# Kernel optimization log

Measured on AMD Instinct MI355X. Metric: run time of the kernel, lower is better.

The kernel has to match this reference:

```python
import jax, jax.numpy as jnp
import numpy as np
import math

INNER = 96
EPS = 1e-8  # torch CosineSimilarity eps


def _proj(x, W1, W2):
    # nn.Linear(C,C,bias=False) -> ReLU -> nn.Linear(C,inner,bias=False)
    return jax.nn.relu(x @ W1) @ W2


def _cos(a, b):
    # torch CosineSimilarity(dim=-1): dot / (max(||a||,eps)*max(||b||,eps))
    num = jnp.sum(a * b, axis=-1)
    na = jnp.maximum(jnp.linalg.norm(a, axis=-1), EPS)
    nb = jnp.maximum(jnp.linalg.norm(b, axis=-1), EPS)
    return num / (na * nb)


def setup_inputs() -> dict:
    key = jax.random.key(0)
    ks = jax.random.split(key, 8)
    B, C, H, W = 128, 768, 7, 7
    sc1 = 1.0 / math.sqrt(C)
    inp = {
        "features_a": jax.random.normal(ks[0], (B, C, H, W), jnp.float32),
        "features_b": jax.random.normal(ks[1], (B, C, H, W), jnp.float32),
        "Wq1": jax.random.normal(ks[2], (C, C), jnp.float32) * sc1,
        "Wq2": jax.random.normal(ks[3], (C, INNER), jnp.float32) * sc1,
        "Wk1": jax.random.normal(ks[4], (C, C), jnp.float32) * sc1,
        "Wk2": jax.random.normal(ks[5], (C, INNER), jnp.float32) * sc1,
        "Wv1": jax.random.normal(ks[6], (C, C), jnp.float32) * sc1,
        "Wv2": jax.random.normal(ks[7], (C, INNER), jnp.float32) * sc1,
    }
    return inp


def reference(features_a, features_b, Wq1, Wq2, Wk1, Wk2, Wv1, Wv2):
    B, C = features_a.shape[0], features_a.shape[1]
    # [B, C, H, W] -> [B, S, C]
    fa = features_a.reshape(B, C, -1).transpose(0, 2, 1)
    fb = features_b.reshape(features_b.shape[0], C, -1).transpose(0, 2, 1)

    qa, ka, va = _proj(fa, Wq1, Wq2), _proj(fa, Wk1, Wk2), _proj(fa, Wv1, Wv2)
    qb, kb, vb = _proj(fb, Wq1, Wq2), _proj(fb, Wk1, Wk2), _proj(fb, Wv1, Wv2)

    scale = 1.0 / math.sqrt(INNER)

    # query_b vs key_a: [Bb, Ba, Sq, Sk]
    scores_ba = jnp.einsum('bqe,ake->baqk', qb, ka) * scale
    probs_ba = jax.nn.softmax(scores_ba, axis=-1)
    aligned_a = jnp.einsum('baqk,ake->baqe', probs_ba, va)  # [Bb, Ba, S, inner]

    # query_a vs key_b: [Bb, Ba, Sq, Sk]
    scores_ab = jnp.einsum('aqe,bke->baqk', qa, kb) * scale
    probs_ab = jax.nn.softmax(scores_ab, axis=-1)
    aligned_b = jnp.einsum('baqk,bke->baqe', probs_ab, vb)  # [Bb, Ba, S, inner]

    sim = _cos(va[None, :, :, :], aligned_b) + _cos(vb[:, None, :, :], aligned_a)
    return sim.mean(-1)  # [Bb, Ba]
```

## Files before the change

kernel.cpp:

```cpp
#include <hip/hip_runtime.h>
#include <hip/hip_bf16.h>
#include <math.h>

typedef __attribute__((ext_vector_type(8))) short bf16x8;
typedef __attribute__((ext_vector_type(4))) float f32x4;

#define MROWS 12544
#define CDIM 768
#define INNER 96
#define S49 49
#define NSIDE 6272
#define SCALE 0.10206207261596577f
#define SCALE_EXP2 ((float)(0.10206207261596577 * 1.4426950408889634))

__device__ __forceinline__ unsigned short f2bf(float f) {
  union { float f; unsigned u; } v; v.f = f;
  unsigned u = v.u;
  return (unsigned short)((u + 0x7fffu + ((u >> 16) & 1u)) >> 16);
}
__device__ __forceinline__ float bf2f(unsigned short h) {
  union { unsigned u; float f; } v; v.u = ((unsigned)h) << 16;
  return v.f;
}
__device__ __forceinline__ unsigned pack_bf16_rn(float a, float b) {
  union { float f; unsigned u; } ua, ub; ua.f = a; ub.f = b;
  return __builtin_amdgcn_perm(ub.u + 0x8000u, ua.u + 0x8000u, 0x07060302u);
}

__device__ __forceinline__ void gld16(const unsigned short* g, unsigned short* l) {
  __builtin_amdgcn_global_load_lds(
      (const __attribute__((address_space(1))) unsigned int*)(g),
      (__attribute__((address_space(3))) unsigned int*)(l), 16, 0, 0);
}

__global__ __launch_bounds__(256) void prep_all(
    const float* __restrict__ fa, const float* __restrict__ fb,
    const float* __restrict__ w10, const float* __restrict__ w11,
    const float* __restrict__ w12, const float* __restrict__ w20,
    const float* __restrict__ w21, const float* __restrict__ w22,
    unsigned short* __restrict__ X,
    unsigned short* __restrict__ W1T, unsigned short* __restrict__ W2T,
    unsigned short* __restrict__ VtKpad) {
  const int t = threadIdx.x;
  int id = blockIdx.x;
  if (id < 3072) {
    __shared__ float T[64][50];
    const int z = id / 1536; id -= z * 1536;
    const int ct = id % 12, img = id / 12;
    const float* feat = z ? fb : fa;
    const float* src = feat + (size_t)img * (CDIM * S49) + (size_t)ct * 64 * S49;
    for (int idx = t; idx < 64 * S49; idx += 256) {
      int cc = idx / S49, s = idx - cc * S49;
      T[cc][s] = src[cc * S49 + s];
    }
    __syncthreads();
    unsigned short* dst = X + (size_t)(z * 128 + img) * S49 * CDIM + ct * 64;
    for (int idx = t; idx < S49 * 64; idx += 256) {
      int s = idx >> 6, cc = idx & 63;
      dst[(size_t)s * CDIM + cc] = f2bf(T[cc][s]);
    }
  } else if (id < 5016) {
    __shared__ float T[32][33];
    id -= 3072;
    const float* src;
    unsigned short* dst;
    int C, ctile, rtile;
    if (id < 1728) {
      int wdx = id / 576, tid = id - wdx * 576;
      ctile = tid % 24; rtile = tid / 24;
      src = wdx == 0 ? w10 : (wdx == 1 ? w11 : w12);
      dst = W1T + (size_t)wdx * CDIM * CDIM;
      C = CDIM;
    } else {
      id -= 1728;
      int wdx = id / 72, tid = id - wdx * 72;
      ctile = tid % 3; rtile = tid / 3;
      src = wdx == 0 ? w20 : (wdx == 1 ? w21 : w22);
      dst = W2T + (size_t)wdx * INNER * CDIM;
      C = INNER;
    }
    const int c0 = ctile * 32, r0 = rtile * 32;
    for (int idx = t; idx < 1024; idx += 256) {
      int rr = idx >> 5, cc = idx & 31;
      T[rr][cc] = src[(size_t)(r0 + rr) * C + c0 + cc];
    }
    __syncthreads();
    for (int idx = t; idx < 1024; idx += 256) {
      int rr = idx >> 5, cc = idx & 31;
      dst[(size_t)(c0 + rr) * CDIM + r0 + cc] = f2bf(T[cc][rr]);
    }
  } else {
    id -= 5016;
    ushort4* p4 = (ushort4*)VtKpad;
    const ushort4 z = make_ushort4(0, 0, 0, 0);
#pragma unroll
    for (int i = 0; i < 32; i++)
      p4[(size_t)id * 8192 + i * 256 + t] = z;
  }
}

__global__ __launch_bounds__(512) void gemm1b4(const unsigned short* __restrict__ X,
                                               const unsigned short* __restrict__ W1T,
                                               unsigned short* __restrict__ H,
                                               int wbase, int hsel) {
  __shared__ __align__(16) unsigned short As[128 * 64];
  __shared__ __align__(16) unsigned short Bs[128 * 64];
  const int t = threadIdx.x;
  const int lane = t & 63, w = t >> 6;
  const int lr = lane & 15, lq = lane >> 4;
  const int wm = w & 3;
  const int wn = w >> 2;
  const int m0 = blockIdx.y * 128, n0 = blockIdx.x * 128;
  const int wdx = blockIdx.z + wbase;
  const unsigned short* W1w = W1T + (size_t)wdx * CDIM * CDIM;
  unsigned short* Hw = H + (hsel ? (size_t)wdx * MROWS * CDIM : 0);
  const f32x4 z4 = {0.f, 0.f, 0.f, 0.f};
  f32x4 acc[2][4] = {{z4, z4, z4, z4}, {z4, z4, z4, z4}};

  for (int k0 = 0; k0 < CDIM; k0 += 64) {
    __syncthreads();
#pragma unroll
    for (int j = 0; j < 2; j++) {
      int idx = t + j * 512;
      int row = idx >> 3, col = (idx & 7) * 8;
      gld16(X + (size_t)(m0 + row) * CDIM + k0 + col, As + idx * 8);
      gld16(W1w + (size_t)(n0 + row) * CDIM + k0 + col, Bs + idx * 8);
    }
    __syncthreads();
#pragma unroll
    for (int ks = 0; ks < 2; ks++) {
      bf16x8 a[2], b[4];
#pragma unroll
      for (int mt = 0; mt < 2; mt++)
        a[mt] = *(const bf16x8*)(As + (wm * 32 + mt * 16 + lr) * 64 + ks * 32 + lq * 8);
#pragma unroll
      for (int nt = 0; nt < 4; nt++)
        b[nt] = *(const bf16x8*)(Bs + (wn * 64 + nt * 16 + lr) * 64 + ks * 32 + lq * 8);
#pragma unroll
      for (int mt = 0; mt < 2; mt++)
#pragma unroll
        for (int nt = 0; nt < 4; nt++)
          acc[mt][nt] = __builtin_amdgcn_mfma_f32_16x16x32_bf16(a[mt], b[nt], acc[mt][nt], 0, 0, 0);
    }
  }
#pragma unroll
  for (int mt = 0; mt < 2; mt++)
#pragma unroll
    for (int nt = 0; nt < 4; nt++)
#pragma unroll
      for (int r = 0; r < 4; r++) {
        int m = m0 + wm * 32 + mt * 16 + lq * 4 + r;
        int n = n0 + wn * 64 + nt * 16 + lr;
        Hw[(size_t)m * CDIM + n] = f2bf(fmaxf(acc[mt][nt][r], 0.f));
      }
}

#define LDK 72
__global__ __launch_bounds__(256) void gemm2b3(const unsigned short* __restrict__ H,
                                               const unsigned short* __restrict__ W2T,
                                               unsigned short* __restrict__ QKV,
                                               unsigned short* __restrict__ Kpad,
                                               unsigned short* __restrict__ Vt,
                                               float* __restrict__ vnorm,
                                               int wbase, int hsel) {
  __shared__ __align__(16) unsigned short As[64 * LDK];
  __shared__ __align__(16) unsigned short Bs[96 * LDK];
  const int t = threadIdx.x;
  const int lane = t & 63, w = t >> 6;
  const int lr = lane & 15, lq = lane >> 4;
  const int m0 = blockIdx.x * 64;
  const int wdx = blockIdx.y + wbase;
  const unsigned short* Hw = H + (hsel ? (size_t)wdx * MROWS * CDIM : 0);
  const unsigned short* W2w = W2T + (size_t)wdx * INNER * CDIM;
  const f32x4 z4 = {0.f, 0.f, 0.f, 0.f};
  f32x4 acc[6] = {z4, z4, z4, z4, z4, z4};

  for (int k0 = 0; k0 < CDIM; k0 += 64) {
    __syncthreads();
    for (int c = t; c < 512; c += 256) {
      int r = c >> 3, kc = (c & 7) * 8;
      *(uint4*)(As + r * LDK + kc) = *(const uint4*)(Hw + (size_t)(m0 + r) * CDIM + k0 + kc);
    }
    for (int c = t; c < 768; c += 256) {
      int r = c >> 3, kc = (c & 7) * 8;
      *(uint4*)(Bs + r * LDK + kc) = *(const uint4*)(W2w + (size_t)r * CDIM + k0 + kc);
    }
    __syncthreads();
#pragma unroll
    for (int kk = 0; kk < 2; kk++) {
      bf16x8 a = *(const bf16x8*)(As + (w * 16 + lr) * LDK + kk * 32 + lq * 8);
#pragma unroll
      for (int nt = 0; nt < 6; nt++) {
        bf16x8 b = *(const bf16x8*)(Bs + (nt * 16 + lr) * LDK + kk * 32 + lq * 8);
        acc[nt] = __builtin_amdgcn_mfma_f32_16x16x32_bf16(a, b, acc[nt], 0, 0, 0);
      }
    }
  }
  float nsq[4] = {0.f, 0.f, 0.f, 0.f};
#pragma unroll
  for (int nt = 0; nt < 6; nt++)
#pragma unroll
    for (int r = 0; r < 4; r++) {
      int m = m0 + w * 16 + lq * 4 + r;
      int e = nt * 16 + lr;
      float v = acc[nt][r];
      int img = m / 49, s = m - img * 49;
      if (wdx == 0) {
        QKV[(size_t)m * INNER + e] = f2bf(v * SCALE_EXP2);
      } else if (wdx == 1) {
        Kpad[(size_t)(img * 64 + s) * INNER + e] = f2bf(v);
      } else {
        QKV[(size_t)(2 * MROWS + m) * INNER + e] = f2bf(v);
        Vt[(size_t)img * (INNER * 64) + e * 64 + s] = f2bf(v);
        nsq[r] += v * v;
      }
    }
  if (wdx == 2) {
#pragma unroll
    for (int r = 0; r < 4; r++) {
      float p = nsq[r];
      p += __shfl_xor(p, 1, 16);
      p += __shfl_xor(p, 2, 16);
      p += __shfl_xor(p, 4, 16);
      p += __shfl_xor(p, 8, 16);
      if (lr == 0) vnorm[m0 + w * 16 + lq * 4 + r] = sqrtf(p);
    }
  }
}

__global__ __launch_bounds__(256) void attn9(const unsigned short* __restrict__ Qp,
                                             const unsigned short* __restrict__ Kpad,
                                             const unsigned short* __restrict__ V,
                                             const unsigned short* __restrict__ Vt,
                                             const float* __restrict__ vnorm,
                                             float* __restrict__ cosbuf) {
  __shared__ __align__(16) unsigned short KsD[2][64 * INNER];
  __shared__ __align__(16) unsigned short VtS[INNER * 64];
  __shared__ __align__(16) unsigned short Ps[4][32 * 64];

  const int t = threadIdx.x;
  const int lane = t & 63, w = t >> 6;
  const int lr = lane & 15, lq = lane >> 4;
  const f32x4 z4 = {0.f, 0.f, 0.f, 0.f};

  int bx = blockIdx.x;
  const int dir = bx / 392; bx -= dir * 392;
  const int chunk = bx >> 3, fg = bx & 7;
  const int r0 = chunk * 128;
  const int qbase = dir * NSIDE;

  int goK[3], goV[3], lo[3];
#pragma unroll
  for (int j = 0; j < 3; j++) {
    int l = (w * 3 + j) * 64 + lane;
    lo[j] = l * 8;
    int rK = l / 12, scK = l - rK * 12;
    int ccK = scK - ((rK >> 1) & 7); if (ccK < 0) ccK += 12;
    goK[j] = rK * INNER + ccK * 8;
    int rV = l >> 3, scV = l & 7;
    int ccV = (scV - (rV & 7)) & 7;
    goV[j] = rV * 64 + ccV * 8;
  }
  int rdK[3], rdV[2];
#pragma unroll
  for (int ks = 0; ks < 3; ks++) {
    int sc = (ks * 4 + lq + ((lr >> 1) & 7)) % 12;
    rdK[ks] = lr * INNER + sc * 8;
  }
#pragma unroll
  for (int ks = 0; ks < 2; ks++) {
    int sc = (ks * 4 + lq + (lr & 7)) & 7;
    rdV[ks] = lr * 64 + sc * 8;
  }

  bf16x8 qf[2][3];
#pragma unroll
  for (int qt = 0; qt < 2; qt++) {
    const int qrow = qbase + r0 + w * 32 + qt * 16 + lr;
#pragma unroll
    for (int ks = 0; ks < 3; ks++)
      qf[qt][ks] = *(const bf16x8*)(Qp + (size_t)qrow * INNER + ks * 32 + lq * 8);
  }
  float rv[2][6][4], invvn[2];
#pragma unroll
  for (int qt = 0; qt < 2; qt++) {
    const int qrow = qbase + r0 + w * 32 + qt * 16 + lr;
    invvn[qt] = 1.f / fmaxf(vnorm[qrow], 1e-8f);
#pragma unroll
    for (int et = 0; et < 6; et++) {
      ushort4 u = *(const ushort4*)(V + (size_t)qrow * INNER + et * 16 + lq * 4);
      rv[qt][et][0] = bf2f(u.x); rv[qt][et][1] = bf2f(u.y);
      rv[qt][et][2] = bf2f(u.z); rv[qt][et][3] = bf2f(u.w);
    }
  }

  unsigned short* Pw = &Ps[w][0];
  const int kimg0 = (dir == 0 ? 128 : 0) + fg * 16;
  {
    const unsigned short* kg = Kpad + (size_t)kimg0 * (64 * INNER);
#pragma unroll
    for (int j = 0; j < 3; j++) gld16(kg + goK[j], &KsD[0][0] + lo[j]);
  }
  for (int fi = 0; fi < 16; fi++) {
    const int f = fg * 16 + fi;
    __syncthreads();
    {
      const unsigned short* vg = Vt + (size_t)(kimg0 + fi) * (INNER * 64);
#pragma unroll
      for (int j = 0; j < 3; j++) gld16(vg + goV[j], VtS + lo[j]);
    }
    const unsigned short* KsC = &KsD[fi & 1][0];
    f32x4 s4[2][4] = {{z4, z4, z4, z4}, {z4, z4, z4, z4}};
#pragma unroll
    for (int ks = 0; ks < 3; ks++) {
#pragma unroll
      for (int kt = 0; kt < 4; kt++) {
        bf16x8 a = *(const bf16x8*)(KsC + kt * (16 * INNER) + rdK[ks]);
        s4[0][kt] = __builtin_amdgcn_mfma_f32_16x16x32_bf16(a, qf[0][ks], s4[0][kt], 0, 0, 0);
        s4[1][kt] = __builtin_amdgcn_mfma_f32_16x16x32_bf16(a, qf[1][ks], s4[1][kt], 0, 0, 0);
      }
    }
#pragma unroll
    for (int qt = 0; qt < 2; qt++)
#pragma unroll
      for (int kt = 0; kt < 4; kt++) {
        float e0 = __builtin_exp2f(s4[qt][kt][0]);
        float e1 = __builtin_exp2f(s4[qt][kt][1]);
        float e2 = __builtin_exp2f(s4[qt][kt][2]);
        float e3 = __builtin_exp2f(s4[qt][kt][3]);
        uint2 pk = make_uint2(pack_bf16_rn(e0, e1), pack_bf16_rn(e2, e3));
        int row = qt * 16 + lr;
        int ch = (2 * kt + (lq >> 1)) ^ (row & 7);
        *(uint2*)(Pw + row * 64 + ch * 8 + (lq & 1) * 4) = pk;
      }
    __syncthreads();
    if (fi < 15) {
      const unsigned short* kg = Kpad + (size_t)(kimg0 + fi + 1) * (64 * INNER);
      unsigned short* kd = &KsD[1 - (fi & 1)][0];
#pragma unroll
      for (int j = 0; j < 3; j++) gld16(kg + goK[j], kd + lo[j]);
    }
    f32x4 pv[2][6] = {{z4, z4, z4, z4, z4, z4}, {z4, z4, z4, z4, z4, z4}};
#pragma unroll
    for (int ks = 0; ks < 2; ks++) {
      int row0 = 0 * 16 + lr, row1 = 1 * 16 + lr;
      int ch0 = ((ks * 4 + lq) ^ (row0 & 7));
      int ch1 = ((ks * 4 + lq) ^ (row1 & 7));
      bf16x8 b0 = *(const bf16x8*)(Pw + row0 * 64 + ch0 * 8);
      bf16x8 b1 = *(const bf16x8*)(Pw + row1 * 64 + ch1 * 8);
#pragma unroll
      for (int et = 0; et < 6; et++) {
        bf16x8 a = *(const bf16x8*)(VtS + et * (16 * 64) + rdV[ks]);
        pv[0][et] = __builtin_amdgcn_mfma_f32_16x16x32_bf16(a, b0, pv[0][et], 0, 0, 0);
        pv[1][et] = __builtin_amdgcn_mfma_f32_16x16x32_bf16(a, b1, pv[1][et], 0, 0, 0);
      }
    }
#pragma unroll
    for (int qt = 0; qt < 2; qt++) {
      float d = 0.f, nn = 0.f;
#pragma unroll
      for (int et = 0; et < 6; et++)
#pragma unroll
        for (int r = 0; r < 4; r++) {
          float al = pv[qt][et][r];
          d += al * rv[qt][et][r];
          nn += al * al;
        }
      d += __shfl_xor(d, 16, 64);  d += __shfl_xor(d, 32, 64);
      nn += __shfl_xor(nn, 16, 64); nn += __shfl_xor(nn, 32, 64);
      if (lane < 16) {
        float cv = d * __frsqrt_rn(fmaxf(nn, 1e-40f)) * invvn[qt];
        cosbuf[(size_t)(dir * 128 + f) * NSIDE + r0 + w * 32 + qt * 16 + lr] = cv;
      }
    }
  }
}

__global__ __launch_bounds__(256) void reduce_out(const float* __restrict__ cosbuf,
                                                  float* __restrict__ out) {
  const int t = threadIdx.x, lane = t & 63, wv = t >> 6;
  const int pair = blockIdx.x * 4 + wv;
  const int bb = pair >> 7, aa = pair & 127;
  float v = 0.f;
  if (lane < S49) {
    v  = cosbuf[(size_t)bb * NSIDE + aa * S49 + lane];
    v += cosbuf[(size_t)(128 + aa) * NSIDE + bb * S49 + lane];
  }
  for (int m = 1; m < 64; m <<= 1) v += __shfl_xor(v, m, 64);
  if (lane == 0) out[pair] = v * (1.f / 49.f);
}

extern "C" void kernel_launch(void* const* d_in, const int* in_sizes, int n_in,
                              void* d_out, int out_size, void* d_ws, size_t ws_size,
                              hipStream_t stream) {
  const float* fa  = (const float*)d_in[0];
  const float* fb  = (const float*)d_in[1];
  const float* W1[3] = {(const float*)d_in[2], (const float*)d_in[4], (const float*)d_in[6]};
  const float* W2[3] = {(const float*)d_in[3], (const float*)d_in[5], (const float*)d_in[7]};
  float* out = (float*)d_out;

  unsigned short* p = (unsigned short*)d_ws;
  unsigned short* Xbf = p;                 p += (size_t)MROWS * CDIM;
  unsigned short* W1T = p;                 p += (size_t)3 * CDIM * CDIM;
  unsigned short* W2T = p;                 p += (size_t)3 * INNER * CDIM;
  unsigned short* QKV = p;                 p += (size_t)3 * MROWS * INNER;
  unsigned short* Vt  = p;                 p += (size_t)256 * INNER * 64;
  unsigned short* Kpad = p;                p += (size_t)256 * 64 * INNER;
  float* vnorm = (float*)p;                p += (size_t)MROWS * 2;
  float* cosbuf = (float*)p;               p += (size_t)256 * NSIDE * 2;
  unsigned short* H = p;                   p += (size_t)3 * MROWS * CDIM;
  const size_t need_batched = (size_t)(p - (unsigned short*)d_ws) * 2;
  const int batched = ws_size >= need_batched;

  prep_all<<<dim3(5112), 256, 0, stream>>>(fa, fb, W1[0], W1[1], W1[2],
                                           W2[0], W2[1], W2[2],
                                           Xbf, W1T, W2T, Vt );
  if (batched) {
    gemm1b4<<<dim3(CDIM / 128, MROWS / 128, 3), 512, 0, stream>>>(Xbf, W1T, H, 0, 1);
    gemm2b3<<<dim3(MROWS / 64, 3), 256, 0, stream>>>(H, W2T, QKV, Kpad, Vt, vnorm, 0, 1);
  } else {
    for (int wdx = 0; wdx < 3; wdx++) {
      gemm1b4<<<dim3(CDIM / 128, MROWS / 128, 1), 512, 0, stream>>>(Xbf, W1T, H, wdx, 0);
      gemm2b3<<<dim3(MROWS / 64, 1), 256, 0, stream>>>(H, W2T, QKV, Kpad, Vt, vnorm, wdx, 0);
    }
  }
  attn9<<<dim3(2 * 392), 256, 0, stream>>>(
      QKV, Kpad, QKV + (size_t)2 * MROWS * INNER, Vt, vnorm, cosbuf);
  reduce_out<<<dim3(4096), 256, 0, stream>>>(cosbuf, out);
}
```

Before: 304.5 us.

## Load V fragments directly from global, drop V LDS stage, double block count

The attention kernel no longer stages V^T in shared memory. Each lane now reads its V MFMA fragments straight from global memory into registers while the softmax exponentials run. The K prefetch for the next image moves to the top of the loop, which removes one __syncthreads per iteration. Each block now covers 8 key images instead of 16, doubling the grid to 1568 blocks, and the kernel adds occupancy launch bounds and s_setprio around the MFMA sections. The risk is higher global/L2 traffic for V, since all four waves reread the same data, plus more Q/V register reloads per block.

Measured after the change: 568.7 us. 86.7% more time.

```diff
diff --git a/kernel.cpp b/kernel.cpp
--- a/kernel.cpp
+++ b/kernel.cpp
@@ -228,14 +228,13 @@
   }
 }
 
-__global__ __launch_bounds__(256) void attn9(const unsigned short* __restrict__ Qp,
-                                             const unsigned short* __restrict__ Kpad,
-                                             const unsigned short* __restrict__ V,
-                                             const unsigned short* __restrict__ Vt,
-                                             const float* __restrict__ vnorm,
-                                             float* __restrict__ cosbuf) {
+__global__ __launch_bounds__(256, 4) void attn10(const unsigned short* __restrict__ Qp,
+                                                 const unsigned short* __restrict__ Kpad,
+                                                 const unsigned short* __restrict__ V,
+                                                 const unsigned short* __restrict__ Vt,
+                                                 const float* __restrict__ vnorm,
+                                                 float* __restrict__ cosbuf) {
   __shared__ __align__(16) unsigned short KsD[2][64 * INNER];
-  __shared__ __align__(16) unsigned short VtS[INNER * 64];
   __shared__ __align__(16) unsigned short Ps[4][32 * 64];
 
   const int t = threadIdx.x;
@@ -244,12 +243,12 @@
   const f32x4 z4 = {0.f, 0.f, 0.f, 0.f};
 
   int bx = blockIdx.x;
-  const int dir = bx / 392; bx -= dir * 392;
-  const int chunk = bx >> 3, fg = bx & 7;
+  const int dir = bx / 784; bx -= dir * 784;
+  const int chunk = bx >> 4, fg = bx & 15;
   const int r0 = chunk * 128;
   const int qbase = dir * NSIDE;
 
-  int goK[3], goV[3], lo[3];
+  int goK[3], lo[3];
 #pragma unroll
   for (int j = 0; j < 3; j++) {
     int l = (w * 3 + j) * 64 + lane;
@@ -257,20 +256,12 @@
     int rK = l / 12, scK = l - rK * 12;
     int ccK = scK - ((rK >> 1) & 7); if (ccK < 0) ccK += 12;
     goK[j] = rK * INNER + ccK * 8;
-    int rV = l >> 3, scV = l & 7;
-    int ccV = (scV - (rV & 7)) & 7;
-    goV[j] = rV * 64 + ccV * 8;
-  }
-  int rdK[3], rdV[2];
+  }
+  int rdK[3];
 #pragma unroll
   for (int ks = 0; ks < 3; ks++) {
     int sc = (ks * 4 + lq + ((lr >> 1) & 7)) % 12;
     rdK[ks] = lr * INNER + sc * 8;
-  }
-#pragma unroll
-  for (int ks = 0; ks < 2; ks++) {
-    int sc = (ks * 4 + lq + (lr & 7)) & 7;
-    rdV[ks] = lr * 64 + sc * 8;
   }
 
   bf16x8 qf[2][3];
@@ -295,22 +286,25 @@
   }
 
   unsigned short* Pw = &Ps[w][0];
-  const int kimg0 = (dir == 0 ? 128 : 0) + fg * 16;
+  const int kimg0 = (dir == 0 ? 128 : 0) + fg * 8;
+  const unsigned short* vbase = Vt + (size_t)kimg0 * (INNER * 64) + lr * 64 + lq * 8;
+
   {
     const unsigned short* kg = Kpad + (size_t)kimg0 * (64 * INNER);
 #pragma unroll
     for (int j = 0; j < 3; j++) gld16(kg + goK[j], &KsD[0][0] + lo[j]);
   }
-  for (int fi = 0; fi < 16; fi++) {
-    const int f = fg * 16 + fi;
-    __syncthreads();
-    {
-      const unsigned short* vg = Vt + (size_t)(kimg0 + fi) * (INNER * 64);
-#pragma unroll
-      for (int j = 0; j < 3; j++) gld16(vg + goV[j], VtS + lo[j]);
+  for (int fi = 0; fi < 8; fi++) {
+    __syncthreads();
+    if (fi < 7) {
+      const unsigned short* kg = Kpad + (size_t)(kimg0 + fi + 1) * (64 * INNER);
+      unsigned short* kd = &KsD[1 - (fi & 1)][0];
+#pragma unroll
+      for (int j = 0; j < 3; j++) gld16(kg + goK[j], kd + lo[j]);
     }
     const unsigned short* KsC = &KsD[fi & 1][0];
     f32x4 s4[2][4] = {{z4, z4, z4, z4}, {z4, z4, z4, z4}};
+    __builtin_amdgcn_s_setprio(1);
 #pragma unroll
     for (int ks = 0; ks < 3; ks++) {
 #pragma unroll
@@ -320,6 +314,11 @@
         s4[1][kt] = __builtin_amdgcn_mfma_f32_16x16x32_bf16(a, qf[1][ks], s4[1][kt], 0, 0, 0);
       }
     }
+    __builtin_amdgcn_s_setprio(0);
+    const unsigned short* vg = vbase + (size_t)fi * (INNER * 64);
+    bf16x8 vf0[6];
+#pragma unroll
+    for (int et = 0; et < 6; et++) vf0[et] = *(const bf16x8*)(vg + et * 1024);
 #pragma unroll
     for (int qt = 0; qt < 2; qt++)
 #pragma unroll
@@ -333,28 +332,34 @@
         int ch = (2 * kt + (lq >> 1)) ^ (row & 7);
         *(uint2*)(Pw + row * 64 + ch * 8 + (lq & 1) * 4) = pk;
       }
-    __syncthreads();
-    if (fi < 15) {
-      const unsigned short* kg = Kpad + (size_t)(kimg0 + fi + 1) * (64 * INNER);
-      unsigned short* kd = &KsD[1 - (fi & 1)][0];
-#pragma unroll
-      for (int j = 0; j < 3; j++) gld16(kg + goK[j], kd + lo[j]);
-    }
     f32x4 pv[2][6] = {{z4, z4, z4, z4, z4, z4}, {z4, z4, z4, z4, z4, z4}};
-#pragma unroll
-    for (int ks = 0; ks < 2; ks++) {
-      int row0 = 0 * 16 + lr, row1 = 1 * 16 + lr;
-      int ch0 = ((ks * 4 + lq) ^ (row0 & 7));
-      int ch1 = ((ks * 4 + lq) ^ (row1 & 7));
-      bf16x8 b0 = *(const bf16x8*)(Pw + row0 * 64 + ch0 * 8);
-      bf16x8 b1 = *(const bf16x8*)(Pw + row1 * 64 + ch1 * 8);
+    bf16x8 vf1[6];
+#pragma unroll
+    for (int et = 0; et < 6; et++) vf1[et] = *(const bf16x8*)(vg + et * 1024 + 32);
+    __builtin_amdgcn_s_setprio(1);
+    {
+      int ch0 = (0 * 4 + lq) ^ (lr & 7);
+      int ch1 = (0 * 4 + lq) ^ ((16 + lr) & 7);
+      bf16x8 b0 = *(const bf16x8*)(Pw + lr * 64 + ch0 * 8);
+      bf16x8 b1 = *(const bf16x8*)(Pw + (16 + lr) * 64 + ch1 * 8);
 #pragma unroll
       for (int et = 0; et < 6; et++) {
-        bf16x8 a = *(const bf16x8*)(VtS + et * (16 * 64) + rdV[ks]);
-        pv[0][et] = __builtin_amdgcn_mfma_f32_16x16x32_bf16(a, b0, pv[0][et], 0, 0, 0);
-        pv[1][et] = __builtin_amdgcn_mfma_f32_16x16x32_bf16(a, b1, pv[1][et], 0, 0, 0);
-      }
-    }
+        pv[0][et] = __builtin_amdgcn_mfma_f32_16x16x32_bf16(vf0[et], b0, pv[0][et], 0, 0, 0);
+        pv[1][et] = __builtin_amdgcn_mfma_f32_16x16x32_bf16(vf0[et], b1, pv[1][et], 0, 0, 0);
+      }
+    }
+    {
+      int ch0 = (1 * 4 + lq) ^ (lr & 7);
+      int ch1 = (1 * 4 + lq) ^ ((16 + lr) & 7);
+      bf16x8 b0 = *(const bf16x8*)(Pw + lr * 64 + ch0 * 8);
+      bf16x8 b1 = *(const bf16x8*)(Pw + (16 + lr) * 64 + ch1 * 8);
+#pragma unroll
+      for (int et = 0; et < 6; et++) {
+        pv[0][et] = __builtin_amdgcn_mfma_f32_16x16x32_bf16(vf1[et], b0, pv[0][et], 0, 0, 0);
+        pv[1][et] = __builtin_amdgcn_mfma_f32_16x16x32_bf16(vf1[et], b1, pv[1][et], 0, 0, 0);
+      }
+    }
+    __builtin_amdgcn_s_setprio(0);
 #pragma unroll
     for (int qt = 0; qt < 2; qt++) {
       float d = 0.f, nn = 0.f;
@@ -370,7 +375,7 @@
       nn += __shfl_xor(nn, 16, 64); nn += __shfl_xor(nn, 32, 64);
       if (lane < 16) {
         float cv = d * __frsqrt_rn(fmaxf(nn, 1e-40f)) * invvn[qt];
-        cosbuf[(size_t)(dir * 128 + f) * NSIDE + r0 + w * 32 + qt * 16 + lr] = cv;
+        cosbuf[(size_t)(dir * 128 + fg * 8 + fi) * NSIDE + r0 + w * 32 + qt * 16 + lr] = cv;
       }
     }
   }
@@ -424,7 +429,7 @@
       gemm2b3<<<dim3(MROWS / 64, 1), 256, 0, stream>>>(H, W2T, QKV, Kpad, Vt, vnorm, wdx, 0);
     }
   }
-  attn9<<<dim3(2 * 392), 256, 0, stream>>>(
+  attn10<<<dim3(2 * 784), 256, 0, stream>>>(
       QKV, Kpad, QKV + (size_t)2 * MROWS * INNER, Vt, vnorm, cosbuf);
   reduce_out<<<dim3(4096), 256, 0, stream>>>(cosbuf, out);
 }
```
